# Performance work log

Hardware: AMD Instinct MI355X
Metric: run time of the kernel (lower is better)

Reference implementation:

```python
import jax, jax.numpy as jnp
import numpy as np

N = 50000
EPS = 1e-5


def _layernorm(x, g, b):
    mu = jnp.mean(x, axis=-1, keepdims=True)
    var = jnp.mean((x - mu) ** 2, axis=-1, keepdims=True)
    return (x - mu) * jax.lax.rsqrt(var + EPS) * g + b


def _gcn_conv(x, W, b, src, dst, norm, n):
    # PyG GCNConv: x' = D^{-1/2}(A+I)D^{-1/2} (x W) + b, self-loops already in src/dst
    xw = x @ W                                   # [N, F_out]
    msg = xw[src] * norm[:, None]                # gather + scale, [E+N, F_out]
    return jax.ops.segment_sum(msg, dst, num_segments=n) + b


def _prep_edges(edge_index, n):
    loops = jnp.arange(n, dtype=edge_index.dtype)
    src = jnp.concatenate([edge_index[0], loops])
    dst = jnp.concatenate([edge_index[1], loops])
    deg = jax.ops.segment_sum(jnp.ones(dst.shape[0], jnp.float32), dst, num_segments=n)
    dinv = jnp.where(deg > 0, jax.lax.rsqrt(deg), 0.0)
    norm = dinv[src] * dinv[dst]
    return src, dst, norm


def setup_inputs() -> dict:
    key = jax.random.key(0)
    ks = jax.random.split(key, 8)
    gene, hid, nc = 512, 256, 4
    x = jax.random.normal(ks[0], (N, gene), jnp.float32)
    edge_index = jax.random.randint(ks[1], (2, 1600000), 0, N, dtype=jnp.int64)

    def lin(k, fi, fo):
        return jax.random.normal(k, (fi, fo), jnp.float32) / np.sqrt(fi)

    d = {
        "x": x, "edge_index": edge_index,
        "W1": lin(ks[2], gene, hid), "b1": jnp.zeros(hid, jnp.float32),
        "W2": lin(ks[3], hid, 2 * hid), "b2": jnp.zeros(2 * hid, jnp.float32),
        "W3": lin(ks[4], 2 * hid, hid), "b3": jnp.zeros(hid, jnp.float32),
        "W4": lin(ks[5], hid, hid // 2), "b4": jnp.zeros(hid // 2, jnp.float32),
        "Wc": lin(ks[6], hid // 2, nc), "bc": jnp.zeros(nc, jnp.float32),
        "g1": jnp.ones(hid, jnp.float32), "be1": jnp.zeros(hid, jnp.float32),
        "g2": jnp.ones(2 * hid, jnp.float32), "be2": jnp.zeros(2 * hid, jnp.float32),
        "g3": jnp.ones(hid, jnp.float32), "be3": jnp.zeros(hid, jnp.float32),
        "g4": jnp.ones(hid // 2, jnp.float32), "be4": jnp.zeros(hid // 2, jnp.float32),
    }
    return d


def reference(x, edge_index, W1, b1, W2, b2, W3, b3, W4, b4, Wc, bc,
              g1, be1, g2, be2, g3, be3, g4, be4):
    n = x.shape[0]
    src, dst, norm = _prep_edges(edge_index, n)
    # dropout layers are identity (training=False)
    h1 = jax.nn.elu(_layernorm(_gcn_conv(x, W1, b1, src, dst, norm, n), g1, be1))
    h2 = jax.nn.elu(_layernorm(_gcn_conv(h1, W2, b2, src, dst, norm, n), g2, be2))
    h3 = jax.nn.elu(_layernorm(_gcn_conv(h2, W3, b3, src, dst, norm, n), g3, be3))
    h4_in = h3 + h1
    out_conv = _gcn_conv(h4_in, W4, b4, src, dst, norm, n)
    out_bn = _layernorm(out_conv, g4, be4)
    h = jax.nn.elu(out_bn)
    return (h @ Wc + bc, out_conv, out_bn)
```

## Files before the change

kernel.cpp:

```cpp
#include <hip/hip_runtime.h>
#include <hip/hip_bf16.h>
#include <math.h>

typedef unsigned short u16;
typedef u16 us8 __attribute__((ext_vector_type(8)));
typedef u16 us4 __attribute__((ext_vector_type(4)));
typedef float f32x4 __attribute__((ext_vector_type(4)));
typedef float f32x8 __attribute__((ext_vector_type(8)));
typedef __bf16 bf8 __attribute__((ext_vector_type(8)));

#define SCAN_B 256
#define CH 8192

__device__ __forceinline__ float bf2f(u16 v) {
    unsigned u = ((unsigned)v) << 16;
    return __builtin_bit_cast(float, u);
}
__device__ __forceinline__ u16 f2bf(float f) {
    unsigned u = __builtin_bit_cast(unsigned, f);
    unsigned lsb = (u >> 16) & 1;
    u += 0x7fff + lsb;
    return (u16)(u >> 16);
}
__device__ __forceinline__ void fma8(f32x8& acc, float w, us8 v) {
#pragma unroll
    for (int j = 0; j < 8; j++) acc[j] += w * bf2f(v[j]);
}

__global__ void detect_k(const int* __restrict__ ei, int E,
                         const u16* __restrict__ xraw, int* flag) {
    __shared__ int c_i32, c_f32;
    if (threadIdx.x == 0) { c_i32 = 0; c_f32 = 0; }
    __syncthreads();
    int ne = (E < 4096) ? E : 4096;
    for (int e = threadIdx.x; e < ne; e += blockDim.x)
        if (ei[2 * e + 1] != 0) c_i32 = 1;
    for (int k = threadIdx.x; k < 8192; k += blockDim.x) {
        u16 v = xraw[2 * k];
        int ex = (v >> 7) & 0xFF;
        if (ex >= 0xF0) atomicAdd(&c_f32, 1);
    }
    __syncthreads();
    if (threadIdx.x == 0) {
        flag[0] = (c_i32 == 0) ? 1 : 0;
        flag[1] = (c_f32 >= 4) ? 1 : 0;
    }
}

__global__ void cvt_x_k(const void* __restrict__ src, u16* __restrict__ dst,
                        long nq, const int* __restrict__ flag) {
    int f32m = flag[1];
    long i0 = (long)blockIdx.x * blockDim.x + threadIdx.x;
    long stride = (long)gridDim.x * blockDim.x;
    if (f32m) {
        const f32x4* s = (const f32x4*)src;
        for (long i = i0; i < nq; i += stride) {
            f32x4 v = s[i];
            us4 o;
            #pragma unroll
            for (int j = 0; j < 4; j++) o[j] = f2bf(v[j]);
            ((us4*)dst)[i] = o;
        }
    } else {
        const us4* s = (const us4*)src;
        for (long i = i0; i < nq; i += stride) ((us4*)dst)[i] = s[i];
    }
}

__global__ void cvt_wt_k(const void* __restrict__ W, u16* __restrict__ Wt,
                         int K, int Nn, const int* __restrict__ flag) {
    int t = blockIdx.x * blockDim.x + threadIdx.x;
    if (t >= K * Nn) return;
    int k = t / Nn, nn = t - k * Nn;
    u16 b;
    if (flag[1]) b = f2bf(((const float*)W)[t]);
    else         b = ((const u16*)W)[t];
    Wt[nn * K + k] = b;
}

struct PEnt { const void* s; int n; int off; };
struct PTab { PEnt e[14]; };
__global__ void cvt_params_k(PTab tab, float* __restrict__ pbuf,
                             const int* __restrict__ flag) {
    PEnt en = tab.e[blockIdx.x];
    int f32m = flag[1];
    for (int i = threadIdx.x; i < en.n; i += blockDim.x) {
        float v = f32m ? ((const float*)en.s)[i] : bf2f(((const u16*)en.s)[i]);
        pbuf[en.off + i] = v;
    }
}

__global__ void init_counts_k(int* counts, int n) {
    int i = blockIdx.x * blockDim.x + threadIdx.x;
    if (i < n) counts[i] = 1;
}

__global__ void histA_k(const int* __restrict__ ei, const int* __restrict__ flag,
                        int* __restrict__ hist, int E, int n, int NB, int NBUK, int shiftv) {
    __shared__ int lh[256];
    int blk = blockIdx.x;
    for (int b = threadIdx.x; b < NBUK; b += 256) lh[b] = 0;
    __syncthreads();
    int e0 = blk * CH;
    int e1 = min(e0 + CH, E);
    int i64 = flag[0];
    for (int e = e0 + threadIdx.x; e < e1; e += 256) {
        int d;
        if (i64) d = (int)((const long long*)ei)[(size_t)E + e];
        else     d = ei[(size_t)E + e];
        int b = ((unsigned)d < (unsigned)n) ? min(d >> shiftv, NBUK - 1) : (NBUK - 1);
        atomicAdd(&lh[b], 1);
    }
    __syncthreads();
    for (int b = threadIdx.x; b < NBUK; b += 256) hist[b * NB + blk] = lh[b];
}

__global__ void scan1_k(const int* __restrict__ counts, int* incl, int* bsum, int n) {
    __shared__ int tmp[SCAN_B];
    int t = threadIdx.x;
    int i = blockIdx.x * SCAN_B + t;
    int v = (i < n) ? counts[i] : 0;
    tmp[t] = v;
    __syncthreads();
    for (int o = 1; o < SCAN_B; o <<= 1) {
        int x = 0;
        if (t >= o) x = tmp[t - o];
        __syncthreads();
        if (t >= o) tmp[t] += x;
        __syncthreads();
    }
    if (i < n) incl[i] = tmp[t];
    if (t == SCAN_B - 1) bsum[blockIdx.x] = tmp[t];
}

__global__ void scan2_k(const int* __restrict__ bsum, int* bscan, int nb) {
    __shared__ int tmp[SCAN_B];
    int t = threadIdx.x;
    tmp[t] = (t < nb) ? bsum[t] : 0;
    __syncthreads();
    for (int o = 1; o < SCAN_B; o <<= 1) {
        int x = 0;
        if (t >= o) x = tmp[t - o];
        __syncthreads();
        if (t >= o) tmp[t] += x;
        __syncthreads();
    }
    bscan[t] = tmp[t];
}

__global__ void exclA_k(const int* __restrict__ incl, const int* __restrict__ bscan,
                        const int* __restrict__ hist, int* __restrict__ ofs, int len) {
    int i = blockIdx.x * 256 + threadIdx.x;
    if (i < len) {
        int boff = (blockIdx.x > 0) ? bscan[blockIdx.x - 1] : 0;
        ofs[i] = incl[i] + boff - hist[i];
    }
}

__global__ void scatC_k(const int* __restrict__ ei, const int* __restrict__ flag,
                        const int* __restrict__ ofs, long long* __restrict__ ebuf,
                        int E, int n, int NB, int NBUK, int shiftv) {
    __shared__ int cur[256];
    int blk = blockIdx.x;
    for (int b = threadIdx.x; b < NBUK; b += 256) cur[b] = ofs[b * NB + blk];
    __syncthreads();
    int e0 = blk * CH;
    int e1 = min(e0 + CH, E);
    int i64 = flag[0];
    for (int e = e0 + threadIdx.x; e < e1; e += 256) {
        int s, d;
        if (i64) {
            const long long* e64 = (const long long*)ei;
            s = (int)e64[e]; d = (int)e64[(size_t)E + e];
        } else {
            s = ei[e]; d = ei[(size_t)E + e];
        }
        int b = ((unsigned)d < (unsigned)n) ? min(d >> shiftv, NBUK - 1) : (NBUK - 1);
        int pos = atomicAdd(&cur[b], 1);
        ebuf[pos] = ((long long)(unsigned)d << 32) | (unsigned)s;
    }
}

__global__ void count_ebuf_k(const long long* __restrict__ ebuf, int* counts, int E, int n) {
    int e = blockIdx.x * blockDim.x + threadIdx.x;
    if (e >= E) return;
    long long pr = ebuf[e];
    int d = (int)(pr >> 32);
    if ((unsigned)d < (unsigned)n) atomicAdd(&counts[d], 1);
}

__global__ void dinv_k(const int* __restrict__ counts, float* dinv, int n) {
    int i = blockIdx.x * blockDim.x + threadIdx.x;
    if (i < n) dinv[i] = rsqrtf((float)counts[i]);
}

__global__ void rowptr_k(const int* __restrict__ incl, const int* __restrict__ bscan,
                         int* rowptr, int n) {
    int i = blockIdx.x * blockDim.x + threadIdx.x;
    if (i < n) {
        int boff = (blockIdx.x > 0) ? bscan[blockIdx.x - 1] : 0;
        rowptr[i + 1] = incl[i] + boff;
        if (i == 0) rowptr[0] = 0;
    }
}

__global__ void cursor_k(const int* __restrict__ rowptr, int* cursor, int n) {
    int i = blockIdx.x * blockDim.x + threadIdx.x;
    if (i < n) cursor[i] = rowptr[i];
}

__global__ void scatD_k(const long long* __restrict__ ebuf, int* cursor,
                        int* __restrict__ col, int E, int n) {
    int e = blockIdx.x * blockDim.x + threadIdx.x;
    if (e < E) {
        long long pr = ebuf[e];
        int d = (int)(pr >> 32);
        int s = (int)(pr & 0xffffffffLL);
        if ((unsigned)s < (unsigned)n && (unsigned)d < (unsigned)n) {
            int pos = atomicAdd(&cursor[d], 1);
            col[pos] = s;
        }
    } else if (e < E + n) {
        int i = e - E;
        int pos = atomicAdd(&cursor[i], 1);
        col[pos] = i;
    }
}

#define TM 64
#define TN 64
#define BK 32
#define LDSS 40

__global__ __launch_bounds__(256) void gemm_bt_k(
    const u16* __restrict__ A, const u16* __restrict__ Bt,
    u16* __restrict__ C, int M, int K, int Nn) {
    __shared__ u16 As[TM * LDSS];
    __shared__ u16 Bs[TN * LDSS];
    int tid = threadIdx.x;
    int wave = tid >> 6;
    int lane = tid & 63;
    int wm = (wave & 1) * 32;
    int wn = (wave >> 1) * 32;
    int row0 = blockIdx.x * TM;
    int col0 = blockIdx.y * TN;

    f32x4 acc00 = {0.f, 0.f, 0.f, 0.f}, acc01 = acc00, acc10 = acc00, acc11 = acc00;

    int lrow = tid >> 2;
    int lcol = (tid & 3) * 8;
    int q = lane >> 4;
    int m = lane & 15;

    for (int k0 = 0; k0 < K; k0 += BK) {
        int gr = row0 + lrow;
        us8 va = (us8)0;
        if (gr < M) va = *(const us8*)(A + (size_t)gr * K + k0 + lcol);
        *(us8*)(&As[lrow * LDSS + lcol]) = va;
        int gc = col0 + lrow;
        us8 vb = (us8)0;
        if (gc < Nn) vb = *(const us8*)(Bt + (size_t)gc * K + k0 + lcol);
        *(us8*)(&Bs[lrow * LDSS + lcol]) = vb;
        __syncthreads();

        us8 a0 = *(const us8*)(&As[(wm + m) * LDSS + q * 8]);
        us8 a1 = *(const us8*)(&As[(wm + 16 + m) * LDSS + q * 8]);
        us8 b0 = *(const us8*)(&Bs[(wn + m) * LDSS + q * 8]);
        us8 b1 = *(const us8*)(&Bs[(wn + 16 + m) * LDSS + q * 8]);
        bf8 fa0 = __builtin_bit_cast(bf8, a0);
        bf8 fa1 = __builtin_bit_cast(bf8, a1);
        bf8 fb0 = __builtin_bit_cast(bf8, b0);
        bf8 fb1 = __builtin_bit_cast(bf8, b1);
        acc00 = __builtin_amdgcn_mfma_f32_16x16x32_bf16(fa0, fb0, acc00, 0, 0, 0);
        acc01 = __builtin_amdgcn_mfma_f32_16x16x32_bf16(fa0, fb1, acc01, 0, 0, 0);
        acc10 = __builtin_amdgcn_mfma_f32_16x16x32_bf16(fa1, fb0, acc10, 0, 0, 0);
        acc11 = __builtin_amdgcn_mfma_f32_16x16x32_bf16(fa1, fb1, acc11, 0, 0, 0);
        __syncthreads();
    }

    int cn = lane & 15;
    #pragma unroll
    for (int r = 0; r < 4; r++) {
        int rr = q * 4 + r;
        int row_a = row0 + wm + rr;
        int row_b = row0 + wm + 16 + rr;
        if (row_a < M) {
            C[(size_t)row_a * Nn + col0 + wn + cn] = f2bf(acc00[r]);
            C[(size_t)row_a * Nn + col0 + wn + 16 + cn] = f2bf(acc01[r]);
        }
        if (row_b < M) {
            C[(size_t)row_b * Nn + col0 + wn + cn] = f2bf(acc10[r]);
            C[(size_t)row_b * Nn + col0 + wn + 16 + cn] = f2bf(acc11[r]);
        }
    }
}

__global__ __launch_bounds__(256) void agg_k(
    const u16* __restrict__ in, const int* __restrict__ rowptr,
    const int* __restrict__ col, const float* __restrict__ dinv,
    const float* __restrict__ bias, const float* __restrict__ gamma,
    const float* __restrict__ beta, u16* __restrict__ out_h,
    const u16* __restrict__ resid, void* __restrict__ final_base,
    const int* __restrict__ flag, const float* __restrict__ Wcf,
    const float* __restrict__ bcf, int F, int nN) {
    int wv = threadIdx.x >> 6;
    int lane = threadIdx.x & 63;
    int i = blockIdx.x * 4 + wv;
    if (i >= nN) return;

    int rowt = F >> 3;
    int Gw = 64 / rowt;
    int g = lane / rowt;
    int f0 = (lane & (rowt - 1)) << 3;

    int beg = rowptr[i], end = rowptr[i + 1];
    f32x8 acc = {0, 0, 0, 0, 0, 0, 0, 0}, acc2 = acc;
    int e = beg + g;
    for (; e + Gw < end; e += 2 * Gw) {
        int s0 = col[e], s1 = col[e + Gw];
        s0 = ((unsigned)s0 < (unsigned)nN) ? s0 : 0;
        s1 = ((unsigned)s1 < (unsigned)nN) ? s1 : 0;
        float w0 = dinv[s0], w1 = dinv[s1];
        us8 v0 = *(const us8*)(in + (unsigned)(s0 * F) + f0);
        us8 v1 = *(const us8*)(in + (unsigned)(s1 * F) + f0);
        fma8(acc, w0, v0);
        fma8(acc2, w1, v1);
    }
    if (e < end) {
        int s = col[e];
        s = ((unsigned)s < (unsigned)nN) ? s : 0;
        us8 v = *(const us8*)(in + (unsigned)(s * F) + f0);
        fma8(acc, dinv[s], v);
    }
    #pragma unroll
    for (int j = 0; j < 8; j++) acc[j] += acc2[j];

    for (int o = 32; o >= rowt; o >>= 1) {
        #pragma unroll
        for (int j = 0; j < 8; j++) acc[j] += __shfl_down(acc[j], o);
    }
    bool active = lane < rowt;
    float di = dinv[i];

    if (!bias) {
        if (active) {
            us8 o8;
            #pragma unroll
            for (int j = 0; j < 8; j++) o8[j] = f2bf(di * acc[j]);
            *(us8*)(out_h + (unsigned)(i * F) + f0) = o8;
        }
        return;
    }

    f32x8 accv = {0, 0, 0, 0, 0, 0, 0, 0};
    if (active) {
        #pragma unroll
        for (int j = 0; j < 8; j++) accv[j] = di * acc[j] + bias[f0 + j];
    }
    int f32m = final_base ? flag[1] : 0;
    if (final_base && active) {
        size_t conv_idx = (size_t)nN * 4 + (size_t)i * F + f0;
        if (f32m) {
            #pragma unroll
            for (int j = 0; j < 8; j++) ((float*)final_base)[conv_idx + j] = accv[j];
        } else {
            us8 o8;
            #pragma unroll
            for (int j = 0; j < 8; j++) o8[j] = f2bf(accv[j]);
            *(us8*)((u16*)final_base + conv_idx) = o8;
        }
    }

    float p1 = 0.f, p2 = 0.f;
    #pragma unroll
    for (int j = 0; j < 8; j++) { p1 += accv[j]; p2 += accv[j] * accv[j]; }
    for (int o = rowt >> 1; o >= 1; o >>= 1) {
        p1 += __shfl_xor(p1, o);
        p2 += __shfl_xor(p2, o);
    }
    float invF = 1.0f / (float)F;
    float mu = p1 * invF;
    float var = fmaxf(p2 * invF - mu * mu, 0.f);
    float rstd = rsqrtf(var + 1e-5f);

    f32x8 h8 = {0, 0, 0, 0, 0, 0, 0, 0};
    if (active) {
        f32x8 y8;
        #pragma unroll
        for (int j = 0; j < 8; j++)
            y8[j] = (accv[j] - mu) * rstd * gamma[f0 + j] + beta[f0 + j];
        if (final_base) {
            size_t bn_idx = (size_t)nN * 4 + (size_t)nN * F + (size_t)i * F + f0;
            if (f32m) {
                #pragma unroll
                for (int j = 0; j < 8; j++) ((float*)final_base)[bn_idx + j] = y8[j];
            } else {
                us8 o8;
                #pragma unroll
                for (int j = 0; j < 8; j++) o8[j] = f2bf(y8[j]);
                *(us8*)((u16*)final_base + bn_idx) = o8;
            }
        }
        #pragma unroll
        for (int j = 0; j < 8; j++) h8[j] = (y8[j] > 0.f) ? y8[j] : expm1f(y8[j]);
        if (resid) {
            us8 r8 = *(const us8*)(resid + (unsigned)(i * F) + f0);
            #pragma unroll
            for (int j = 0; j < 8; j++) h8[j] += bf2f(r8[j]);
        }
        if (out_h) {
            us8 o8;
            #pragma unroll
            for (int j = 0; j < 8; j++) o8[j] = f2bf(h8[j]);
            *(us8*)(out_h + (unsigned)(i * F) + f0) = o8;
        }
    }

    if (Wcf) {
        float s0 = 0.f, s1 = 0.f, s2 = 0.f, s3 = 0.f;
        if (active) {
            #pragma unroll
            for (int j = 0; j < 8; j++) {
                const float* wr = Wcf + (f0 + j) * 4;
                s0 += h8[j] * wr[0];
                s1 += h8[j] * wr[1];
                s2 += h8[j] * wr[2];
                s3 += h8[j] * wr[3];
            }
        }
        for (int o = rowt >> 1; o >= 1; o >>= 1) {
            s0 += __shfl_xor(s0, o);
            s1 += __shfl_xor(s1, o);
            s2 += __shfl_xor(s2, o);
            s3 += __shfl_xor(s3, o);
        }
        if (lane == 0) {
            size_t lidx = (size_t)i * 4;
            if (f32m) {
                ((float*)final_base)[lidx + 0] = s0 + bcf[0];
                ((float*)final_base)[lidx + 1] = s1 + bcf[1];
                ((float*)final_base)[lidx + 2] = s2 + bcf[2];
                ((float*)final_base)[lidx + 3] = s3 + bcf[3];
            } else {
                ((u16*)final_base)[lidx + 0] = f2bf(s0 + bcf[0]);
                ((u16*)final_base)[lidx + 1] = f2bf(s1 + bcf[1]);
                ((u16*)final_base)[lidx + 2] = f2bf(s2 + bcf[2]);
                ((u16*)final_base)[lidx + 3] = f2bf(s3 + bcf[3]);
            }
        }
    }
}

__global__ void ln_elu_k(u16* __restrict__ h, const float* __restrict__ bias,
                         const float* __restrict__ gamma,
                         const float* __restrict__ beta, int F) {
    int i = blockIdx.x;
    int f = threadIdx.x;
    size_t idx = (size_t)i * F + f;
    float v = bf2f(h[idx]) + (bias ? bias[f] : 0.f);
    float p1 = v, p2 = v * v;
    #pragma unroll
    for (int o = 32; o >= 1; o >>= 1) {
        p1 += __shfl_down(p1, o);
        p2 += __shfl_down(p2, o);
    }
    __shared__ float red1[8], red2[8], stats[2];
    int lane = threadIdx.x & 63, w = threadIdx.x >> 6;
    if (lane == 0) { red1[w] = p1; red2[w] = p2; }
    __syncthreads();
    if (threadIdx.x == 0) {
        float t1 = 0.f, t2 = 0.f;
        int nw = blockDim.x >> 6;
        for (int j = 0; j < nw; j++) { t1 += red1[j]; t2 += red2[j]; }
        float invF = 1.0f / (float)F;
        float mu = t1 * invF;
        float var = fmaxf(t2 * invF - mu * mu, 0.f);
        stats[0] = mu;
        stats[1] = rsqrtf(var + 1e-5f);
    }
    __syncthreads();
    float y = (v - stats[0]) * stats[1] * gamma[f] + beta[f];
    float hh = (y > 0.f) ? y : expm1f(y);
    h[idx] = f2bf(hh);
}

__global__ void marker_k(float* out) {
    if (threadIdx.x == 0 && blockIdx.x == 0) {
        out[0] = 31337.0f; out[1] = 31337.0f;
    }
}

extern "C" void kernel_launch(void* const* d_in, const int* in_sizes, int n_in,
                              void* d_out, int out_size, void* d_ws, size_t ws_size,
                              hipStream_t stream) {
    const int N = in_sizes[0] / 512;
    const int E = in_sizes[1] / 2;

    const void* x  = d_in[0];
    const int* ei  = (const int*)d_in[1];

    char* p = (char*)d_ws;
    auto alloc = [&](size_t bytes) -> void* {
        void* r = (void*)p;
        p += (bytes + 255) & ~(size_t)255;
        return r;
    };
    int*   flag   = (int*)alloc(256);
    int*   counts = (int*)alloc((size_t)N * 4);
    int*   rowptr = (int*)alloc((size_t)(N + 1) * 4);
    int*   cursor = (int*)alloc((size_t)N * 4);
    int*   incl   = (int*)alloc((size_t)N * 4);
    int*   bsum   = (int*)alloc(256 * 4);
    int*   bscan  = (int*)alloc(256 * 4);
    float* dinv   = (float*)alloc((size_t)N * 4);
    int*   col    = (int*)alloc((size_t)(E + N) * 4);
    float* pbuf   = (float*)alloc(4096 * 4);
    u16* W1t = (u16*)alloc((size_t)512 * 256 * 2);
    u16* W2t = (u16*)alloc((size_t)256 * 512 * 2);
    u16* W3t = (u16*)alloc((size_t)512 * 256 * 2);
    u16* W4t = (u16*)alloc((size_t)256 * 128 * 2);
    u16* bigA = (u16*)alloc((size_t)N * 512 * 2);
    u16* xw   = (u16*)alloc((size_t)N * 256 * 2);
    u16* h1   = (u16*)alloc((size_t)N * 256 * 2);

    size_t needed = (size_t)(p - (char*)d_ws);
    if (needed > ws_size) {
        marker_k<<<1, 64, 0, stream>>>((float*)d_out);
        return;
    }

    u16* xbf = bigA;
    u16* h2  = bigA;

    int shiftv = 8;
    while (((N - 1) >> shiftv) > 255) shiftv++;
    int NBUK = ((N - 1) >> shiftv) + 1;
    int NB_E = (E + CH - 1) / CH;
    int flatlen = NBUK * NB_E;
    int NH = (flatlen + 255) / 256;
    long long* ebuf = (long long*)xw;
    int* hist     = (int*)h1;
    int* histincl = hist + flatlen;
    int* ofs      = histincl + flatlen;

    PTab tab;
    tab.e[0]  = { d_in[3],  256, 0    };
    tab.e[1]  = { d_in[12], 256, 256  };
    tab.e[2]  = { d_in[13], 256, 512  };
    tab.e[3]  = { d_in[5],  512, 768  };
    tab.e[4]  = { d_in[14], 512, 1280 };
    tab.e[5]  = { d_in[15], 512, 1792 };
    tab.e[6]  = { d_in[7],  256, 2304 };
    tab.e[7]  = { d_in[16], 256, 2560 };
    tab.e[8]  = { d_in[17], 256, 2816 };
    tab.e[9]  = { d_in[9],  128, 3072 };
    tab.e[10] = { d_in[18], 128, 3200 };
    tab.e[11] = { d_in[19], 128, 3328 };
    tab.e[12] = { d_in[10], 512, 3456 };
    tab.e[13] = { d_in[11], 4,   3968 };
    float* b1f = pbuf + 0,   *g1f = pbuf + 256,  *be1f = pbuf + 512;
    float* b2f = pbuf + 768, *g2f = pbuf + 1280, *be2f = pbuf + 1792;
    float* b3f = pbuf + 2304,*g3f = pbuf + 2560, *be3f = pbuf + 2816;
    float* b4f = pbuf + 3072,*g4f = pbuf + 3200, *be4f = pbuf + 3328;
    float* Wcf = pbuf + 3456,*bcf = pbuf + 3968;

    int nb1 = (N + 255) / 256;
    int NB = (N + SCAN_B - 1) / SCAN_B;

    detect_k<<<1, 256, 0, stream>>>(ei, E, (const u16*)x, flag);

    cvt_x_k<<<4096, 256, 0, stream>>>(x, xbf, (long)N * 512 / 4, flag);
    cvt_wt_k<<<(512 * 256 + 255) / 256, 256, 0, stream>>>(d_in[2], W1t, 512, 256, flag);
    cvt_wt_k<<<(256 * 512 + 255) / 256, 256, 0, stream>>>(d_in[4], W2t, 256, 512, flag);
    cvt_wt_k<<<(512 * 256 + 255) / 256, 256, 0, stream>>>(d_in[6], W3t, 512, 256, flag);
    cvt_wt_k<<<(256 * 128 + 255) / 256, 256, 0, stream>>>(d_in[8], W4t, 256, 128, flag);
    cvt_params_k<<<14, 256, 0, stream>>>(tab, pbuf, flag);

    histA_k<<<NB_E, 256, 0, stream>>>(ei, flag, hist, E, N, NB_E, NBUK, shiftv);
    scan1_k<<<NH, SCAN_B, 0, stream>>>(hist, histincl, bsum, flatlen);
    scan2_k<<<1, SCAN_B, 0, stream>>>(bsum, bscan, NH);
    exclA_k<<<NH, 256, 0, stream>>>(histincl, bscan, hist, ofs, flatlen);
    scatC_k<<<NB_E, 256, 0, stream>>>(ei, flag, ofs, ebuf, E, N, NB_E, NBUK, shiftv);
    init_counts_k<<<nb1, 256, 0, stream>>>(counts, N);
    count_ebuf_k<<<(E + 255) / 256, 256, 0, stream>>>(ebuf, counts, E, N);
    dinv_k<<<nb1, 256, 0, stream>>>(counts, dinv, N);
    scan1_k<<<NB, SCAN_B, 0, stream>>>(counts, incl, bsum, N);
    scan2_k<<<1, SCAN_B, 0, stream>>>(bsum, bscan, NB);
    rowptr_k<<<NB, SCAN_B, 0, stream>>>(incl, bscan, rowptr, N);
    cursor_k<<<nb1, 256, 0, stream>>>(rowptr, cursor, N);
    scatD_k<<<(E + N + 255) / 256, 256, 0, stream>>>(ebuf, cursor, col, E, N);

    int gx = (N + TM - 1) / TM;
    int ga = (N + 3) / 4;

    gemm_bt_k<<<dim3(gx, 256 / TN), 256, 0, stream>>>(xbf, W1t, xw, N, 512, 256);
    agg_k<<<ga, 256, 0, stream>>>(xw, rowptr, col, dinv, b1f, g1f, be1f,
                                  h1, nullptr, nullptr, flag, nullptr, nullptr, 256, N);
    agg_k<<<ga, 256, 0, stream>>>(h1, rowptr, col, dinv, nullptr, nullptr, nullptr,
                                  xw, nullptr, nullptr, flag, nullptr, nullptr, 256, N);
    gemm_bt_k<<<dim3(gx, 512 / TN), 256, 0, stream>>>(xw, W2t, h2, N, 256, 512);
    ln_elu_k<<<N, 512, 0, stream>>>(h2, b2f, g2f, be2f, 512);
    gemm_bt_k<<<dim3(gx, 256 / TN), 256, 0, stream>>>(h2, W3t, xw, N, 512, 256);
    agg_k<<<ga, 256, 0, stream>>>(xw, rowptr, col, dinv, b3f, g3f, be3f,
                                  h1, h1, nullptr, flag, nullptr, nullptr, 256, N);
    gemm_bt_k<<<dim3(gx, 128 / TN), 256, 0, stream>>>(h1, W4t, xw, N, 256, 128);
    agg_k<<<ga, 256, 0, stream>>>(xw, rowptr, col, dinv, b4f, g4f, be4f,
                                  nullptr, nullptr, d_out, flag, Wcf, bcf, 128, N);
}
```

Baseline: 989.9 us.

## Use 128x128 MFMA GEMM tiles with direct-to-LDS loads, unroll aggregation, warp-level layernorm

```diff
diff --git a/kernel.cpp b/kernel.cpp
--- a/kernel.cpp
+++ b/kernel.cpp
@@ -227,70 +227,74 @@
     }
 }
 
-#define TM 64
-#define TN 64
-#define BK 32
-#define LDSS 40
-
-__global__ __launch_bounds__(256) void gemm_bt_k(
+typedef __attribute__((address_space(1))) const void gas_v;
+typedef __attribute__((address_space(3))) void las_v;
+
+__global__ __launch_bounds__(256) void gemm128_k(
     const u16* __restrict__ A, const u16* __restrict__ Bt,
     u16* __restrict__ C, int M, int K, int Nn) {
-    __shared__ u16 As[TM * LDSS];
-    __shared__ u16 Bs[TN * LDSS];
+    __shared__ u16 As[128 * 32];
+    __shared__ u16 Bs[128 * 32];
     int tid = threadIdx.x;
     int wave = tid >> 6;
     int lane = tid & 63;
-    int wm = (wave & 1) * 32;
-    int wn = (wave >> 1) * 32;
-    int row0 = blockIdx.x * TM;
-    int col0 = blockIdx.y * TN;
-
-    f32x4 acc00 = {0.f, 0.f, 0.f, 0.f}, acc01 = acc00, acc10 = acc00, acc11 = acc00;
-
-    int lrow = tid >> 2;
-    int lcol = (tid & 3) * 8;
+    int wr = (wave >> 1) * 64;
+    int wc = (wave & 1) * 64;
+    long row0 = (long)blockIdx.x * 128;
+    int col0 = blockIdx.y * 128;
+    int lr = lane >> 2;
+    int lc = lane & 3;
+    int m = lane & 15;
     int q = lane >> 4;
-    int m = lane & 15;
-
-    for (int k0 = 0; k0 < K; k0 += BK) {
-        int gr = row0 + lrow;
-        us8 va = (us8)0;
-        if (gr < M) va = *(const us8*)(A + (size_t)gr * K + k0 + lcol);
-        *(us8*)(&As[lrow * LDSS + lcol]) = va;
-        int gc = col0 + lrow;
-        us8 vb = (us8)0;
-        if (gc < Nn) vb = *(const us8*)(Bt + (size_t)gc * K + k0 + lcol);
-        *(us8*)(&Bs[lrow * LDSS + lcol]) = vb;
+
+    f32x4 acc[4][4];
+    #pragma unroll
+    for (int i = 0; i < 4; i++)
+        #pragma unroll
+        for (int j = 0; j < 4; j++) acc[i][j] = (f32x4){0.f, 0.f, 0.f, 0.f};
+
+    for (int k0 = 0; k0 < K; k0 += 32) {
+        #pragma unroll
+        for (int p = 0; p < 2; p++) {
+            int c = wave + p * 4;
+            long ar = row0 + c * 16 + lr;
+            if (ar > (long)M - 1) ar = (long)M - 1;
+            const u16* ga = A + ar * K + k0 + lc * 8;
+            __builtin_amdgcn_global_load_lds((gas_v*)ga, (las_v*)&As[c * 512], 16, 0, 0);
+            int br = col0 + c * 16 + lr;
+            const u16* gb = Bt + (size_t)br * K + k0 + lc * 8;
+            __builtin_amdgcn_global_load_lds((gas_v*)gb, (las_v*)&Bs[c * 512], 16, 0, 0);
+        }
         __syncthreads();
 
-        us8 a0 = *(const us8*)(&As[(wm + m) * LDSS + q * 8]);
-        us8 a1 = *(const us8*)(&As[(wm + 16 + m) * LDSS + q * 8]);
-        us8 b0 = *(const us8*)(&Bs[(wn + m) * LDSS + q * 8]);
-        us8 b1 = *(const us8*)(&Bs[(wn + 16 + m) * LDSS + q * 8]);
-        bf8 fa0 = __builtin_bit_cast(bf8, a0);
-        bf8 fa1 = __builtin_bit_cast(bf8, a1);
-        bf8 fb0 = __builtin_bit_cast(bf8, b0);
-        bf8 fb1 = __builtin_bit_cast(bf8, b1);
-        acc00 = __builtin_amdgcn_mfma_f32_16x16x32_bf16(fa0, fb0, acc00, 0, 0, 0);
-        acc01 = __builtin_amdgcn_mfma_f32_16x16x32_bf16(fa0, fb1, acc01, 0, 0, 0);
-        acc10 = __builtin_amdgcn_mfma_f32_16x16x32_bf16(fa1, fb0, acc10, 0, 0, 0);
-        acc11 = __builtin_amdgcn_mfma_f32_16x16x32_bf16(fa1, fb1, acc11, 0, 0, 0);
+        us8 av[4], bv[4];
+        #pragma unroll
+        for (int i = 0; i < 4; i++) {
+            av[i] = *(const us8*)&As[(wr + i * 16 + m) * 32 + q * 8];
+            bv[i] = *(const us8*)&Bs[(wc + i * 16 + m) * 32 + q * 8];
+        }
+        #pragma unroll
+        for (int i = 0; i < 4; i++) {
+            bf8 fa = __builtin_bit_cast(bf8, av[i]);
+            #pragma unroll
+            for (int j = 0; j < 4; j++) {
+                bf8 fb = __builtin_bit_cast(bf8, bv[j]);
+                acc[i][j] = __builtin_amdgcn_mfma_f32_16x16x32_bf16(fa, fb, acc[i][j], 0, 0, 0);
+            }
+        }
         __syncthreads();
     }
 
-    int cn = lane & 15;
-    #pragma unroll
-    for (int r = 0; r < 4; r++) {
-        int rr = q * 4 + r;
-        int row_a = row0 + wm + rr;
-        int row_b = row0 + wm + 16 + rr;
-        if (row_a < M) {
-            C[(size_t)row_a * Nn + col0 + wn + cn] = f2bf(acc00[r]);
-            C[(size_t)row_a * Nn + col0 + wn + 16 + cn] = f2bf(acc01[r]);
-        }
-        if (row_b < M) {
-            C[(size_t)row_b * Nn + col0 + wn + cn] = f2bf(acc10[r]);
-            C[(size_t)row_b * Nn + col0 + wn + 16 + cn] = f2bf(acc11[r]);
+    #pragma unroll
+    for (int i = 0; i < 4; i++) {
+        #pragma unroll
+        for (int r = 0; r < 4; r++) {
+            long row = row0 + wr + i * 16 + q * 4 + r;
+            if (row < M) {
+                #pragma unroll
+                for (int j = 0; j < 4; j++)
+                    C[row * Nn + col0 + wc + j * 16 + m] = f2bf(acc[i][j][r]);
+            }
         }
     }
 }
@@ -314,8 +318,24 @@
     int f0 = (lane & (rowt - 1)) << 3;
 
     int beg = rowptr[i], end = rowptr[i + 1];
-    f32x8 acc = {0, 0, 0, 0, 0, 0, 0, 0}, acc2 = acc;
+    f32x8 acc = {0, 0, 0, 0, 0, 0, 0, 0}, acc2 = acc, acc3 = acc, acc4 = acc;
     int e = beg + g;
+    for (; e + 3 * Gw < end; e += 4 * Gw) {
+        int s0 = col[e], s1 = col[e + Gw], s2 = col[e + 2 * Gw], s3 = col[e + 3 * Gw];
+        s0 = ((unsigned)s0 < (unsigned)nN) ? s0 : 0;
+        s1 = ((unsigned)s1 < (unsigned)nN) ? s1 : 0;
+        s2 = ((unsigned)s2 < (unsigned)nN) ? s2 : 0;
+        s3 = ((unsigned)s3 < (unsigned)nN) ? s3 : 0;
+        float w0 = dinv[s0], w1 = dinv[s1], w2 = dinv[s2], w3 = dinv[s3];
+        us8 v0 = *(const us8*)(in + (unsigned)(s0 * F) + f0);
+        us8 v1 = *(const us8*)(in + (unsigned)(s1 * F) + f0);
+        us8 v2 = *(const us8*)(in + (unsigned)(s2 * F) + f0);
+        us8 v3 = *(const us8*)(in + (unsigned)(s3 * F) + f0);
+        fma8(acc, w0, v0);
+        fma8(acc2, w1, v1);
+        fma8(acc3, w2, v2);
+        fma8(acc4, w3, v3);
+    }
     for (; e + Gw < end; e += 2 * Gw) {
         int s0 = col[e], s1 = col[e + Gw];
         s0 = ((unsigned)s0 < (unsigned)nN) ? s0 : 0;
@@ -333,7 +353,7 @@
         fma8(acc, dinv[s], v);
     }
     #pragma unroll
-    for (int j = 0; j < 8; j++) acc[j] += acc2[j];
+    for (int j = 0; j < 8; j++) acc[j] = (acc[j] + acc2[j]) + (acc3[j] + acc4[j]);
 
     for (int o = 32; o >= rowt; o >>= 1) {
         #pragma unroll
@@ -451,37 +471,40 @@
     }
 }
 
-__global__ void ln_elu_k(u16* __restrict__ h, const float* __restrict__ bias,
-                         const float* __restrict__ gamma,
-                         const float* __restrict__ beta, int F) {
-    int i = blockIdx.x;
-    int f = threadIdx.x;
-    size_t idx = (size_t)i * F + f;
-    float v = bf2f(h[idx]) + (bias ? bias[f] : 0.f);
-    float p1 = v, p2 = v * v;
+__global__ __launch_bounds__(256) void ln_elu_k(u16* __restrict__ h,
+                                                const float* __restrict__ bias,
+                                                const float* __restrict__ gamma,
+                                                const float* __restrict__ beta, int nN) {
+    int wv = threadIdx.x >> 6;
+    int lane = threadIdx.x & 63;
+    int i = blockIdx.x * 4 + wv;
+    if (i >= nN) return;
+    int f0 = lane * 8;
+    size_t base = (size_t)i * 512 + f0;
+    us8 v8 = *(const us8*)(h + base);
+    f32x8 v;
+    #pragma unroll
+    for (int j = 0; j < 8; j++) v[j] = bf2f(v8[j]) + bias[f0 + j];
+    float p1 = 0.f, p2 = 0.f;
+    #pragma unroll
+    for (int j = 0; j < 8; j++) { p1 += v[j]; p2 += v[j] * v[j]; }
     #pragma unroll
     for (int o = 32; o >= 1; o >>= 1) {
-        p1 += __shfl_down(p1, o);
-        p2 += __shfl_down(p2, o);
-    }
-    __shared__ float red1[8], red2[8], stats[2];
-    int lane = threadIdx.x & 63, w = threadIdx.x >> 6;
-    if (lane == 0) { red1[w] = p1; red2[w] = p2; }
-    __syncthreads();
-    if (threadIdx.x == 0) {
-        float t1 = 0.f, t2 = 0.f;
-        int nw = blockDim.x >> 6;
-        for (int j = 0; j < nw; j++) { t1 += red1[j]; t2 += red2[j]; }
-        float invF = 1.0f / (float)F;
-        float mu = t1 * invF;
-        float var = fmaxf(t2 * invF - mu * mu, 0.f);
-        stats[0] = mu;
-        stats[1] = rsqrtf(var + 1e-5f);
-    }
-    __syncthreads();
-    float y = (v - stats[0]) * stats[1] * gamma[f] + beta[f];
-    float hh = (y > 0.f) ? y : expm1f(y);
-    h[idx] = f2bf(hh);
+        p1 += __shfl_xor(p1, o);
+        p2 += __shfl_xor(p2, o);
+    }
+    const float invF = 1.0f / 512.0f;
+    float mu = p1 * invF;
+    float var = fmaxf(p2 * invF - mu * mu, 0.f);
+    float rstd = rsqrtf(var + 1e-5f);
+    us8 o8;
+    #pragma unroll
+    for (int j = 0; j < 8; j++) {
+        float y = (v[j] - mu) * rstd * gamma[f0 + j] + beta[f0 + j];
+        y = (y > 0.f) ? y : expm1f(y);
+        o8[j] = f2bf(y);
+    }
+    *(us8*)(h + base) = o8;
 }
 
 __global__ void marker_k(float* out) {
@@ -590,20 +613,20 @@
     cursor_k<<<nb1, 256, 0, stream>>>(rowptr, cursor, N);
     scatD_k<<<(E + N + 255) / 256, 256, 0, stream>>>(ebuf, cursor, col, E, N);
 
-    int gx = (N + TM - 1) / TM;
+    int gx = (N + 127) / 128;
     int ga = (N + 3) / 4;
 
-    gemm_bt_k<<<dim3(gx, 256 / TN), 256, 0, stream>>>(xbf, W1t, xw, N, 512, 256);
+    gemm128_k<<<dim3(gx, 256 / 128), 256, 0, stream>>>(xbf, W1t, xw, N, 512, 256);
     agg_k<<<ga, 256, 0, stream>>>(xw, rowptr, col, dinv, b1f, g1f, be1f,
                                   h1, nullptr, nullptr, flag, nullptr, nullptr, 256, N);
     agg_k<<<ga, 256, 0, stream>>>(h1, rowptr, col, dinv, nullptr, nullptr, nullptr,
                                   xw, nullptr, nullptr, flag, nullptr, nullptr, 256, N);
-    gemm_bt_k<<<dim3(gx, 512 / TN), 256, 0, stream>>>(xw, W2t, h2, N, 256, 512);
-    ln_elu_k<<<N, 512, 0, stream>>>(h2, b2f, g2f, be2f, 512);
-    gemm_bt_k<<<dim3(gx, 256 / TN), 256, 0, stream>>>(h2, W3t, xw, N, 512, 256);
+    gemm128_k<<<dim3(gx, 512 / 128), 256, 0, stream>>>(xw, W2t, h2, N, 256, 512);
+    ln_elu_k<<<ga, 256, 0, stream>>>(h2, b2f, g2f, be2f, N);
+    gemm128_k<<<dim3(gx, 256 / 128), 256, 0, stream>>>(h2, W3t, xw, N, 512, 256);
     agg_k<<<ga, 256, 0, stream>>>(xw, rowptr, col, dinv, b3f, g3f, be3f,
                                   h1, h1, nullptr, flag, nullptr, nullptr, 256, N);
-    gemm_bt_k<<<dim3(gx, 128 / TN), 256, 0, stream>>>(h1, W4t, xw, N, 256, 128);
+    gemm128_k<<<dim3(gx, 128 / 128), 256, 0, stream>>>(h1, W4t, xw, N, 256, 128);
     agg_k<<<ga, 256, 0, stream>>>(xw, rowptr, col, dinv, b4f, g4f, be4f,
                                   nullptr, nullptr, d_out, flag, Wcf, bcf, 128, N);
 }
```

Result: no change. 1.003 ms (+1.3%).
